# Kernel tuning notes

Measured on AMD Instinct MI355X. Metric: run time of the kernel, lower is better.

Reference implementation:

```python
import jax, jax.numpy as jnp
import numpy as np

N_NODES = 50000
N_EDGES = 1000000
N_QUERY = 100000
NUM_FEATURES = 256
HIDDEN = 256
LABEL_DIM = 2


def glorot(key, shape):
    lim = float(np.sqrt(6.0 / (shape[0] + shape[1])))
    return jax.random.uniform(key, shape, jnp.float32, -lim, lim)


def setup_inputs() -> dict:
    key = jax.random.key(0)
    ks = jax.random.split(key, 8)
    x = jax.random.normal(ks[0], (N_NODES, NUM_FEATURES), jnp.float32)
    edge_index = jax.random.randint(ks[1], (2, N_EDGES), 0, N_NODES)
    query_edges = jax.random.randint(ks[2], (N_QUERY, 2), 0, N_NODES)
    edge_weight = jax.random.uniform(ks[3], (N_EDGES,), jnp.float32)
    W1 = glorot(ks[4], (NUM_FEATURES, HIDDEN))
    b1 = jnp.zeros((HIDDEN,), jnp.float32)
    W2 = glorot(ks[5], (HIDDEN, HIDDEN))
    b2 = jnp.zeros((HIDDEN,), jnp.float32)
    Wl = glorot(ks[6], (2 * HIDDEN, LABEL_DIM))
    bl = jnp.zeros((LABEL_DIM,), jnp.float32)
    return {"x": x, "edge_index": edge_index, "query_edges": query_edges,
            "edge_weight": edge_weight, "W1": W1, "b1": b1, "W2": W2,
            "b2": b2, "Wl": Wl, "bl": bl}


def digcn_conv(x, edge_index, edge_weight, W, b):
    # x: [N, F_in] -> h: [N, F_out]; propagate: out[dst] += w_e * h[src]
    h = x @ W
    src, dst = edge_index[0], edge_index[1]
    msg = h[src] * edge_weight[:, None]            # [E, F_out]
    agg = jax.ops.segment_sum(msg, dst, num_segments=x.shape[0])
    return agg + b


def reference(x, edge_index, query_edges, edge_weight, W1, b1, W2, b2, Wl, bl):
    h = jax.nn.relu(digcn_conv(x, edge_index, edge_weight, W1, b1))
    # dropout is identity at eval time
    h = digcn_conv(h, edge_index, edge_weight, W2, b2)
    q = jnp.concatenate((h[query_edges[:, 0]], h[query_edges[:, 1]]), axis=-1)
    logits = q @ Wl + bl
    return jax.nn.log_softmax(logits, axis=1)
```

## Files before the change

kernel.cpp:

```cpp
#include <hip/hip_runtime.h>
#include <hip/hip_bf16.h>
#include <math.h>

typedef __bf16 bf16;
typedef __bf16 v8bf __attribute__((ext_vector_type(8)));
typedef __bf16 v4bf __attribute__((ext_vector_type(4)));
typedef float  v4f  __attribute__((ext_vector_type(4)));

#define FDIM 256
#define BKT_CAP 8192
#define AROW 264
#define GEMM_BLOCKS 512


__global__ __launch_bounds__(256) void flag_kernel(float* __restrict__ out, int n) {
  int i = blockIdx.x * 256 + threadIdx.x;
  if (i < n) out[i] = 1.0e9f;
}

__global__ __launch_bounds__(256) void k1_prep(const float* __restrict__ W1,
                                               const float* __restrict__ W2,
                                               bf16* __restrict__ Wt1,
                                               bf16* __restrict__ Wt2,
                                               const int* __restrict__ dst,
                                               int* __restrict__ phist,
                                               const float* __restrict__ Wl,
                                               const float* __restrict__ b2,
                                               const float* __restrict__ bl,
                                               float4* __restrict__ V,
                                               float* __restrict__ cc,
                                               int E, int N, int nbkt) {
  __shared__ int h[256];
  __shared__ float sWl[1024];
  __shared__ float red[256];
  int b = blockIdx.x;
  int t = threadIdx.x;
  if (b < 512) {
    const float* W = (b >> 8) ? W2 : W1;
    bf16* Wt = (b >> 8) ? Wt2 : Wt1;
    int k = b & 255;
    Wt[t * FDIM + k] = (bf16)W[k * FDIM + t];
  } else if (b < 768) {
    int pb = b - 512;
    h[t] = 0;
    __syncthreads();
    for (int e = pb * 256 + t; e < E; e += 256 * 256) {
      int d = dst[e];
      d = d < 0 ? 0 : (d >= N ? N - 1 : d);
      atomicAdd(&h[d >> 8], 1);
    }
    __syncthreads();
    phist[pb * 256 + t] = h[t];
  } else {
#pragma unroll
    for (int j = 0; j < 4; ++j) sWl[j * 256 + t] = Wl[j * 256 + t];
    __syncthreads();
    const float* w2row = W2 + (size_t)t * FDIM;
    float4 acc = make_float4(0.f, 0.f, 0.f, 0.f);
    for (int j = 0; j < 256; ++j) {
      float w = w2row[j];
      acc.x += w * sWl[2 * j + 0];
      acc.y += w * sWl[2 * j + 1];
      acc.z += w * sWl[512 + 2 * j + 0];
      acc.w += w * sWl[512 + 2 * j + 1];
    }
    V[t] = acc;
    float bj = b2[t];
    red[t] = bj * (sWl[2 * t + 0] + sWl[512 + 2 * t + 0]);
    __syncthreads();
    if (t == 0) {
      float s = 0.f;
      for (int j = 0; j < 256; ++j) s += red[j];
      cc[0] = s + bl[0];
    }
    __syncthreads();
    red[t] = bj * (sWl[2 * t + 1] + sWl[512 + 2 * t + 1]);
    __syncthreads();
    if (t == 0) {
      float s = 0.f;
      for (int j = 0; j < 256; ++j) s += red[j];
      cc[1] = s + bl[1];
    }
  }
}

__global__ __launch_bounds__(256) void p2_scan(const int* __restrict__ phist,
                                               int* __restrict__ bbase,
                                               int* __restrict__ gcur,
                                               int* __restrict__ offs,
                                               int nbkt, int Nn) {
  __shared__ int wsum[4];
  int t = threadIdx.x, lane = t & 63, wv = t >> 6;
  int v = 0;
  for (int pb = 0; pb < 256; ++pb) v += phist[pb * 256 + t];
  if (t >= nbkt) v = 0;
  int x = v;
#pragma unroll
  for (int d = 1; d < 64; d <<= 1) {
    int y = __shfl_up(x, d, 64);
    if (lane >= d) x += y;
  }
  if (lane == 63) wsum[wv] = x;
  __syncthreads();
  int woff = 0;
  if (wv >= 1) woff += wsum[0];
  if (wv >= 2) woff += wsum[1];
  if (wv >= 3) woff += wsum[2];
  int incl = woff + x;
  int excl = incl - v;
  if (t < nbkt) { bbase[t] = excl; gcur[t] = excl; }
  if (t == 255) {
    bbase[nbkt] = incl;
    offs[Nn] = incl;
  }
}


__device__ inline void stage64(const float* __restrict__ A, bf16* __restrict__ As,
                               int row0, int M, int tid) {
#pragma unroll
  for (int j = 0; j < 8; ++j) {
    int g = j * 2048 + tid * 8;
    int r = g >> 8, c = g & 255;
    int gr = row0 + r; if (gr >= M) gr = M - 1;
    const float* p = A + (size_t)gr * FDIM + c;
    float4 f0 = *reinterpret_cast<const float4*>(p);
    float4 f1 = *reinterpret_cast<const float4*>(p + 4);
    v8bf o;
    o[0] = (bf16)f0.x; o[1] = (bf16)f0.y; o[2] = (bf16)f0.z; o[3] = (bf16)f0.w;
    o[4] = (bf16)f1.x; o[5] = (bf16)f1.y; o[6] = (bf16)f1.z; o[7] = (bf16)f1.w;
    *reinterpret_cast<v8bf*>(As + r * AROW + c) = o;
  }
}

__device__ inline void gemm_body(const float* __restrict__ A, const bf16* __restrict__ Bt,
                                 bf16* __restrict__ C, int M, int bid, int nblocks,
                                 bf16* __restrict__ As) {
  const int K = FDIM, N = FDIM;
  int tid = threadIdx.x;
  int wave = tid >> 6;
  int lane = tid & 63;
  int l15 = lane & 15, quad = lane >> 4;

  v8bf bfr[4][8];
#pragma unroll
  for (int nn = 0; nn < 4; ++nn) {
    const bf16* bp = Bt + (size_t)(wave * 64 + nn * 16 + l15) * K + quad * 8;
#pragma unroll
    for (int kk = 0; kk < 8; ++kk)
      bfr[nn][kk] = *reinterpret_cast<const v8bf*>(bp + kk * 32);
  }

  int ntiles = (M + 63) >> 6;
  for (int tile = bid; tile < ntiles; tile += nblocks) {
    int row0 = tile * 64;
    __syncthreads();
    stage64(A, As, row0, M, tid);
    __syncthreads();

#pragma unroll
    for (int st = 0; st < 4; ++st) {
      v8bf afr[8];
#pragma unroll
      for (int kk = 0; kk < 8; ++kk)
        afr[kk] = *reinterpret_cast<const v8bf*>(As + (st * 16 + l15) * AROW + quad * 8 + kk * 32);

      v4f acc[4];
#pragma unroll
      for (int nn = 0; nn < 4; ++nn) acc[nn] = (v4f){0.f, 0.f, 0.f, 0.f};

#pragma unroll
      for (int kk = 0; kk < 8; ++kk)
#pragma unroll
        for (int nn = 0; nn < 4; ++nn)
          acc[nn] = __builtin_amdgcn_mfma_f32_16x16x32_bf16(afr[kk], bfr[nn][kk], acc[nn], 0, 0, 0);

#pragma unroll
      for (int nn = 0; nn < 4; ++nn)
#pragma unroll
        for (int r = 0; r < 4; ++r) {
          int row = row0 + st * 16 + quad * 4 + r;
          int col = wave * 64 + nn * 16 + l15;
          if (row < M) C[(size_t)row * N + col] = (bf16)acc[nn][r];
        }
    }
  }
}

__device__ inline void p3_body(const int* __restrict__ src, const int* __restrict__ dst,
                               const float* __restrict__ ew, int* __restrict__ gcur,
                               uint2* __restrict__ tmp, int E, int N, int nbkt,
                               int pb, int nblocks, int* h, int* base, int* cnt) {
  int t = threadIdx.x;
  int chunk = (E + nblocks - 1) / nblocks;
  int lo = pb * chunk;
  int hi = lo + chunk; if (hi > E) hi = E;
  h[t] = 0; cnt[t] = 0;
  __syncthreads();
  for (int e = lo + t; e < hi; e += 256) {
    int d = dst[e];
    d = d < 0 ? 0 : (d >= N ? N - 1 : d);
    atomicAdd(&h[d >> 8], 1);
  }
  __syncthreads();
  if (t < nbkt) base[t] = atomicAdd(&gcur[t], h[t]);
  __syncthreads();
  for (int e = lo + t; e < hi; e += 256) {
    int d = dst[e];
    d = d < 0 ? 0 : (d >= N ? N - 1 : d);
    int b = d >> 8;
    int sv = src[e];
    sv = sv < 0 ? 0 : (sv >= N ? N - 1 : sv);
    unsigned int u = __float_as_uint(ew[e]);
    unsigned int wbits = ((u + 0x7FFFu + ((u >> 16) & 1u)) & 0xFFFF0000u);
    unsigned int meta = wbits | (unsigned int)(sv & 0xFFFF);
    int r = atomicAdd(&cnt[b], 1);
    int pos = base[b] + r;
    if (pos >= 0 && pos < E) tmp[pos] = make_uint2(meta, (unsigned int)d);
  }
}

__global__ __launch_bounds__(256, 2) void k3_gemm1_p3(const float* __restrict__ x,
                                                      const bf16* __restrict__ Wt1,
                                                      bf16* __restrict__ bufT, int M,
                                                      const int* __restrict__ src,
                                                      const int* __restrict__ dst,
                                                      const float* __restrict__ ew,
                                                      int* __restrict__ gcur,
                                                      uint2* __restrict__ tmp,
                                                      int E, int N, int nbkt) {
  __shared__ bf16 As[64 * AROW];
  __shared__ int h[256], base[256], cnt[256];
  if (blockIdx.x < GEMM_BLOCKS)
    gemm_body(x, Wt1, bufT, M, blockIdx.x, GEMM_BLOCKS, As);
  else
    p3_body(src, dst, ew, gcur, tmp, E, N, nbkt, blockIdx.x - GEMM_BLOCKS, 256, h, base, cnt);
}

__global__ __launch_bounds__(256) void p4_sort(const uint2* __restrict__ tmp,
                                               const int* __restrict__ bbase,
                                               unsigned int* __restrict__ pmeta,
                                               int* __restrict__ offs,
                                               int Nn, int E) {
  __shared__ uint2 ent[BKT_CAP];
  __shared__ int h2[256], ex2[256], c2[256];
  __shared__ int wsum[4];
  int b = blockIdx.x, t = threadIdx.x, lane = t & 63, wv = t >> 6;
  int s0 = bbase[b], s1 = bbase[b + 1];
  int count = s1 - s0;
  if (count < 0) count = 0;
  if (count > BKT_CAP) count = BKT_CAP;
  for (int i = t; i < count; i += 256) ent[i] = tmp[s0 + i];
  h2[t] = 0; c2[t] = 0;
  __syncthreads();
  for (int i = t; i < count; i += 256) atomicAdd(&h2[ent[i].y & 255u], 1);
  __syncthreads();
  int v = h2[t];
  int x = v;
#pragma unroll
  for (int d = 1; d < 64; d <<= 1) {
    int y = __shfl_up(x, d, 64);
    if (lane >= d) x += y;
  }
  if (lane == 63) wsum[wv] = x;
  __syncthreads();
  int woff = 0;
  if (wv >= 1) woff += wsum[0];
  if (wv >= 2) woff += wsum[1];
  if (wv >= 3) woff += wsum[2];
  int excl = woff + x - v;
  ex2[t] = excl;
  int node = (b << 8) + t;
  if (node < Nn) offs[node] = s0 + excl;
  __syncthreads();
  for (int i = t; i < count; i += 256) {
    int l = (int)(ent[i].y & 255u);
    int r = atomicAdd(&c2[l], 1);
    int pos = s0 + ex2[l] + r;
    if (pos >= 0 && pos < E) pmeta[pos] = ent[i].x;
  }
}

__global__ __launch_bounds__(256) void agg1G(const bf16* __restrict__ T,
                                             const unsigned int* __restrict__ pmeta,
                                             const int* __restrict__ offsets,
                                             const float* __restrict__ bias,
                                             const float4* __restrict__ V,
                                             float4* __restrict__ G, int N, int E) {
  int node = blockIdx.x * 4 + (threadIdx.x >> 6);
  if (node >= N) return;
  int lane = threadIdx.x & 63;
  int f = lane * 4;
  int beg = offsets[node], end = offsets[node + 1];
  beg = beg < 0 ? 0 : (beg > E ? E : beg);
  end = end < beg ? beg : (end > E ? E : end);
  const unsigned int* m = pmeta + beg;
  int cnt = end - beg;

  float a0 = 0.f, a1 = 0.f, a2 = 0.f, a3 = 0.f;
  int p = 0;
  for (; p + 8 <= cnt; p += 8) {
    unsigned int mv[8];
#pragma unroll
    for (int j = 0; j < 8; ++j) mv[j] = m[p + j];
    v4bf tv[8];
#pragma unroll
    for (int j = 0; j < 8; ++j) {
      int s = (int)(mv[j] & 0xFFFFu);
      s = s >= N ? N - 1 : s;
      tv[j] = *reinterpret_cast<const v4bf*>(T + (size_t)s * FDIM + f);
    }
#pragma unroll
    for (int j = 0; j < 8; ++j) {
      float w = __uint_as_float(mv[j] & 0xFFFF0000u);
      a0 += w * (float)tv[j][0];
      a1 += w * (float)tv[j][1];
      a2 += w * (float)tv[j][2];
      a3 += w * (float)tv[j][3];
    }
  }
  for (; p < cnt; ++p) {
    unsigned int mv = m[p];
    int s = (int)(mv & 0xFFFFu);
    s = s >= N ? N - 1 : s;
    float w = __uint_as_float(mv & 0xFFFF0000u);
    v4bf tv = *reinterpret_cast<const v4bf*>(T + (size_t)s * FDIM + f);
    a0 += w * (float)tv[0];
    a1 += w * (float)tv[1];
    a2 += w * (float)tv[2];
    a3 += w * (float)tv[3];
  }
  a0 = fmaxf(a0 + bias[f + 0], 0.f);
  a1 = fmaxf(a1 + bias[f + 1], 0.f);
  a2 = fmaxf(a2 + bias[f + 2], 0.f);
  a3 = fmaxf(a3 + bias[f + 3], 0.f);

  float4 v0 = V[f + 0], v1 = V[f + 1], v2 = V[f + 2], v3 = V[f + 3];
  float gx = a0 * v0.x + a1 * v1.x + a2 * v2.x + a3 * v3.x;
  float gy = a0 * v0.y + a1 * v1.y + a2 * v2.y + a3 * v3.y;
  float gz = a0 * v0.z + a1 * v1.z + a2 * v2.z + a3 * v3.z;
  float gw = a0 * v0.w + a1 * v1.w + a2 * v2.w + a3 * v3.w;
#pragma unroll
  for (int d = 32; d > 0; d >>= 1) {
    gx += __shfl_down(gx, d, 64);
    gy += __shfl_down(gy, d, 64);
    gz += __shfl_down(gz, d, 64);
    gw += __shfl_down(gw, d, 64);
  }
  if (lane == 0) G[node] = make_float4(gx, gy, gz, gw);
}

__global__ __launch_bounds__(256) void aggP(const float4* __restrict__ G,
                                            const unsigned int* __restrict__ pmeta,
                                            const int* __restrict__ offsets,
                                            float4* __restrict__ P, int N, int E) {
  int node = blockIdx.x * 256 + threadIdx.x;
  if (node >= N) return;
  int beg = offsets[node], end = offsets[node + 1];
  beg = beg < 0 ? 0 : (beg > E ? E : beg);
  end = end < beg ? beg : (end > E ? E : end);
  float ax = 0.f, ay = 0.f, az = 0.f, aw = 0.f;
  int p = beg;
  for (; p + 4 <= end; p += 4) {
    unsigned int m0 = pmeta[p + 0], m1 = pmeta[p + 1], m2 = pmeta[p + 2], m3 = pmeta[p + 3];
    int s0 = (int)(m0 & 0xFFFFu); s0 = s0 >= N ? N - 1 : s0;
    int s1 = (int)(m1 & 0xFFFFu); s1 = s1 >= N ? N - 1 : s1;
    int s2 = (int)(m2 & 0xFFFFu); s2 = s2 >= N ? N - 1 : s2;
    int s3 = (int)(m3 & 0xFFFFu); s3 = s3 >= N ? N - 1 : s3;
    float4 g0 = G[s0], g1 = G[s1], g2 = G[s2], g3 = G[s3];
    float w0 = __uint_as_float(m0 & 0xFFFF0000u);
    float w1 = __uint_as_float(m1 & 0xFFFF0000u);
    float w2 = __uint_as_float(m2 & 0xFFFF0000u);
    float w3 = __uint_as_float(m3 & 0xFFFF0000u);
    ax += w0 * g0.x + w1 * g1.x + w2 * g2.x + w3 * g3.x;
    ay += w0 * g0.y + w1 * g1.y + w2 * g2.y + w3 * g3.y;
    az += w0 * g0.z + w1 * g1.z + w2 * g2.z + w3 * g3.z;
    aw += w0 * g0.w + w1 * g1.w + w2 * g2.w + w3 * g3.w;
  }
  for (; p < end; ++p) {
    unsigned int mm = pmeta[p];
    int s = (int)(mm & 0xFFFFu); s = s >= N ? N - 1 : s;
    float w = __uint_as_float(mm & 0xFFFF0000u);
    float4 g = G[s];
    ax += w * g.x; ay += w * g.y; az += w * g.z; aw += w * g.w;
  }
  P[node] = make_float4(ax, ay, az, aw);
}

__global__ __launch_bounds__(256) void query_small(const int* __restrict__ qe,
                                                   const float4* __restrict__ P,
                                                   const float* __restrict__ cc,
                                                   float* __restrict__ out, int Q, int N) {
  int q = blockIdx.x * 256 + threadIdx.x;
  if (q >= Q) return;
  int n0 = qe[2 * q + 0]; n0 = n0 < 0 ? 0 : (n0 >= N ? N - 1 : n0);
  int n1 = qe[2 * q + 1]; n1 = n1 < 0 ? 0 : (n1 >= N ? N - 1 : n1);
  float4 p0 = P[n0];
  float4 p1 = P[n1];
  float l0 = p0.x + p1.z + cc[0];
  float l1 = p0.y + p1.w + cc[1];
  float m = fmaxf(l0, l1);
  float lse = m + logf(expf(l0 - m) + expf(l1 - m));
  out[2 * q + 0] = l0 - lse;
  out[2 * q + 1] = l1 - lse;
}


extern "C" void kernel_launch(void* const* d_in, const int* in_sizes, int n_in,
                              void* d_out, int out_size, void* d_ws, size_t ws_size,
                              hipStream_t stream) {
  const float* x  = (const float*)d_in[0];
  const int*   ei = (const int*)d_in[1];
  const int*   qe = (const int*)d_in[2];
  const float* ew = (const float*)d_in[3];
  const float* W1 = (const float*)d_in[4];
  const float* b1 = (const float*)d_in[5];
  const float* W2 = (const float*)d_in[6];
  const float* b2 = (const float*)d_in[7];
  const float* Wl = (const float*)d_in[8];
  const float* bl = (const float*)d_in[9];

  int N = in_sizes[0] / FDIM;
  int E = in_sizes[1] / 2;
  int Q = in_sizes[2] / 2;
  const int* srcv = ei;
  const int* dstv = ei + E;
  int nbkt = (N + 255) >> 8;

  size_t off = 0;
  auto alloc = [&](size_t bytes) -> void* {
    void* p = (char*)d_ws + off;
    off += (bytes + 255) & ~(size_t)255;
    return p;
  };
  bf16* bufT  = (bf16*)alloc((size_t)N * FDIM * 2);
  uint2* tmp  = (uint2*)alloc((size_t)E * 8);
  bf16* Wt1   = (bf16*)alloc((size_t)FDIM * FDIM * 2);
  bf16* Wt2   = (bf16*)alloc((size_t)FDIM * FDIM * 2);
  int* offs   = (int*)alloc((size_t)(N + 1) * 4);
  unsigned int* pmeta = (unsigned int*)alloc((size_t)E * 4);
  float4* G   = (float4*)alloc((size_t)N * 16);
  float4* P   = (float4*)alloc((size_t)N * 16);
  float4* V   = (float4*)alloc(256 * 16);
  float* cc   = (float*)alloc(2 * 4);
  int* phist  = (int*)alloc(256 * 256 * 4);
  int* bbase  = (int*)alloc(257 * 4);
  int* gcur   = (int*)alloc(256 * 4);

  if (off > ws_size) {
    flag_kernel<<<(out_size + 255) / 256, 256, 0, stream>>>((float*)d_out, out_size);
    return;
  }

  k1_prep<<<769, 256, 0, stream>>>(W1, W2, Wt1, Wt2, dstv, phist, Wl, b2, bl, V, cc,
                                   E, N, nbkt);
  p2_scan<<<1, 256, 0, stream>>>(phist, bbase, gcur, offs, nbkt, N);
  k3_gemm1_p3<<<GEMM_BLOCKS + 256, 256, 0, stream>>>(x, Wt1, bufT, N,
                                                     srcv, dstv, ew, gcur, tmp, E, N, nbkt);
  p4_sort<<<nbkt, 256, 0, stream>>>(tmp, bbase, pmeta, offs, N, E);

  agg1G<<<(N + 3) / 4, 256, 0, stream>>>(bufT, pmeta, offs, b1, V, G, N, E);

  aggP<<<(N + 255) / 256, 256, 0, stream>>>(G, pmeta, offs, P, N, E);

  query_small<<<(Q + 255) / 256, 256, 0, stream>>>(qe, P, cc, (float*)d_out, Q, N);
}
```

Before: 250.9 us.

## Split agg1G by feature slices with persistent waves and atomic partial reductions

The first-layer aggregation is restructured so each block handles a 32-feature slice (8 slices) over a grid-strided set of nodes. Within a wave, four lane groups split the node's edge list and are combined with shuffles, and partial projections onto V are accumulated into G with float atomics. G is now zeroed inside p4_sort. The intent is to make gathers from the feature table hit a smaller working set per slice, which improves cache locality, and to add edge-level parallelism for each node. In exchange, metadata is re-read 8 times, each node needs four global atomics per slice, and the source-index clamp is dropped.

```diff
diff --git a/kernel.cpp b/kernel.cpp
--- a/kernel.cpp
+++ b/kernel.cpp
@@ -5,6 +5,7 @@
 typedef __bf16 bf16;
 typedef __bf16 v8bf __attribute__((ext_vector_type(8)));
 typedef __bf16 v4bf __attribute__((ext_vector_type(4)));
+typedef __bf16 v2bf __attribute__((ext_vector_type(2)));
 typedef float  v4f  __attribute__((ext_vector_type(4)));
 
 #define FDIM 256
@@ -241,11 +242,14 @@
                                                const int* __restrict__ bbase,
                                                unsigned int* __restrict__ pmeta,
                                                int* __restrict__ offs,
+                                               float4* __restrict__ G,
                                                int Nn, int E) {
   __shared__ uint2 ent[BKT_CAP];
   __shared__ int h2[256], ex2[256], c2[256];
   __shared__ int wsum[4];
   int b = blockIdx.x, t = threadIdx.x, lane = t & 63, wv = t >> 6;
+  int nodez = (b << 8) + t;
+  if (nodez < Nn) G[nodez] = make_float4(0.f, 0.f, 0.f, 0.f);
   int s0 = bbase[b], s1 = bbase[b + 1];
   int count = s1 - s0;
   if (count < 0) count = 0;
@@ -287,67 +291,84 @@
                                              const float* __restrict__ bias,
                                              const float4* __restrict__ V,
                                              float4* __restrict__ G, int N, int E) {
-  int node = blockIdx.x * 4 + (threadIdx.x >> 6);
-  if (node >= N) return;
+  int slice = blockIdx.x & 7;
+  int chunk = blockIdx.x >> 3;
+  int nchunk = gridDim.x >> 3;
+  int wv = threadIdx.x >> 6;
   int lane = threadIdx.x & 63;
-  int f = lane * 4;
-  int beg = offsets[node], end = offsets[node + 1];
-  beg = beg < 0 ? 0 : (beg > E ? E : beg);
-  end = end < beg ? beg : (end > E ? E : end);
-  const unsigned int* m = pmeta + beg;
-  int cnt = end - beg;
-
-  float a0 = 0.f, a1 = 0.f, a2 = 0.f, a3 = 0.f;
-  int p = 0;
-  for (; p + 8 <= cnt; p += 8) {
-    unsigned int mv[8];
-#pragma unroll
-    for (int j = 0; j < 8; ++j) mv[j] = m[p + j];
-    v4bf tv[8];
-#pragma unroll
-    for (int j = 0; j < 8; ++j) {
-      int s = (int)(mv[j] & 0xFFFFu);
-      s = s >= N ? N - 1 : s;
-      tv[j] = *reinterpret_cast<const v4bf*>(T + (size_t)s * FDIM + f);
-    }
-#pragma unroll
-    for (int j = 0; j < 8; ++j) {
-      float w = __uint_as_float(mv[j] & 0xFFFF0000u);
-      a0 += w * (float)tv[j][0];
-      a1 += w * (float)tv[j][1];
-      a2 += w * (float)tv[j][2];
-      a3 += w * (float)tv[j][3];
-    }
-  }
-  for (; p < cnt; ++p) {
-    unsigned int mv = m[p];
-    int s = (int)(mv & 0xFFFFu);
-    s = s >= N ? N - 1 : s;
-    float w = __uint_as_float(mv & 0xFFFF0000u);
-    v4bf tv = *reinterpret_cast<const v4bf*>(T + (size_t)s * FDIM + f);
-    a0 += w * (float)tv[0];
-    a1 += w * (float)tv[1];
-    a2 += w * (float)tv[2];
-    a3 += w * (float)tv[3];
-  }
-  a0 = fmaxf(a0 + bias[f + 0], 0.f);
-  a1 = fmaxf(a1 + bias[f + 1], 0.f);
-  a2 = fmaxf(a2 + bias[f + 2], 0.f);
-  a3 = fmaxf(a3 + bias[f + 3], 0.f);
-
-  float4 v0 = V[f + 0], v1 = V[f + 1], v2 = V[f + 2], v3 = V[f + 3];
-  float gx = a0 * v0.x + a1 * v1.x + a2 * v2.x + a3 * v3.x;
-  float gy = a0 * v0.y + a1 * v1.y + a2 * v2.y + a3 * v3.y;
-  float gz = a0 * v0.z + a1 * v1.z + a2 * v2.z + a3 * v3.z;
-  float gw = a0 * v0.w + a1 * v1.w + a2 * v2.w + a3 * v3.w;
-#pragma unroll
-  for (int d = 32; d > 0; d >>= 1) {
-    gx += __shfl_down(gx, d, 64);
-    gy += __shfl_down(gy, d, 64);
-    gz += __shfl_down(gz, d, 64);
-    gw += __shfl_down(gw, d, 64);
-  }
-  if (lane == 0) G[node] = make_float4(gx, gy, gz, gw);
+  int grp = lane >> 4;
+  int l16 = lane & 15;
+  int f = slice * 32 + l16 * 2;
+  const bf16* Tf = T + f;
+
+  float bb0 = bias[f], bb1 = bias[f + 1];
+  float4 v0 = V[f], v1 = V[f + 1];
+
+  int wid = chunk * 4 + wv;
+  int stride = nchunk * 4;
+  for (int node = wid; node < N; node += stride) {
+    int nb = __builtin_amdgcn_readfirstlane(node);
+    int beg = offsets[nb], end = offsets[nb + 1];
+    beg = beg < 0 ? 0 : (beg > E ? E : beg);
+    end = end < beg ? beg : (end > E ? E : end);
+    int cnt = end - beg;
+    int g0 = (cnt * grp) >> 2;
+    int g1 = (cnt * (grp + 1)) >> 2;
+    const unsigned int* m = pmeta + beg;
+
+    float a0 = 0.f, a1 = 0.f;
+    int p = g0;
+    for (; p + 4 <= g1; p += 4) {
+      unsigned int m0 = __builtin_nontemporal_load(&m[p + 0]);
+      unsigned int m1 = __builtin_nontemporal_load(&m[p + 1]);
+      unsigned int m2 = __builtin_nontemporal_load(&m[p + 2]);
+      unsigned int m3 = __builtin_nontemporal_load(&m[p + 3]);
+      v2bf t0 = *reinterpret_cast<const v2bf*>(Tf + ((size_t)(m0 & 0xFFFFu) << 8));
+      v2bf t1 = *reinterpret_cast<const v2bf*>(Tf + ((size_t)(m1 & 0xFFFFu) << 8));
+      v2bf t2 = *reinterpret_cast<const v2bf*>(Tf + ((size_t)(m2 & 0xFFFFu) << 8));
+      v2bf t3 = *reinterpret_cast<const v2bf*>(Tf + ((size_t)(m3 & 0xFFFFu) << 8));
+      float w0 = __uint_as_float(m0 & 0xFFFF0000u);
+      float w1 = __uint_as_float(m1 & 0xFFFF0000u);
+      float w2 = __uint_as_float(m2 & 0xFFFF0000u);
+      float w3 = __uint_as_float(m3 & 0xFFFF0000u);
+      a0 += w0 * (float)t0[0]; a1 += w0 * (float)t0[1];
+      a0 += w1 * (float)t1[0]; a1 += w1 * (float)t1[1];
+      a0 += w2 * (float)t2[0]; a1 += w2 * (float)t2[1];
+      a0 += w3 * (float)t3[0]; a1 += w3 * (float)t3[1];
+    }
+    for (; p < g1; ++p) {
+      unsigned int mv = __builtin_nontemporal_load(&m[p]);
+      float w = __uint_as_float(mv & 0xFFFF0000u);
+      v2bf tv = *reinterpret_cast<const v2bf*>(Tf + ((size_t)(mv & 0xFFFFu) << 8));
+      a0 += w * (float)tv[0];
+      a1 += w * (float)tv[1];
+    }
+
+    a0 += __shfl_xor(a0, 16, 64); a0 += __shfl_xor(a0, 32, 64);
+    a1 += __shfl_xor(a1, 16, 64); a1 += __shfl_xor(a1, 32, 64);
+
+    float r0 = fmaxf(a0 + bb0, 0.f);
+    float r1 = fmaxf(a1 + bb1, 0.f);
+
+    float gx = r0 * v0.x + r1 * v1.x;
+    float gy = r0 * v0.y + r1 * v1.y;
+    float gz = r0 * v0.z + r1 * v1.z;
+    float gw = r0 * v0.w + r1 * v1.w;
+#pragma unroll
+    for (int d = 1; d < 16; d <<= 1) {
+      gx += __shfl_xor(gx, d, 64);
+      gy += __shfl_xor(gy, d, 64);
+      gz += __shfl_xor(gz, d, 64);
+      gw += __shfl_xor(gw, d, 64);
+    }
+    if (lane == 0) {
+      float* gp = reinterpret_cast<float*>(&G[node]);
+      atomicAdd(gp + 0, gx);
+      atomicAdd(gp + 1, gy);
+      atomicAdd(gp + 2, gz);
+      atomicAdd(gp + 3, gw);
+    }
+  }
 }
 
 __global__ __launch_bounds__(256) void aggP(const float4* __restrict__ G,
@@ -457,9 +478,9 @@
   p2_scan<<<1, 256, 0, stream>>>(phist, bbase, gcur, offs, nbkt, N);
   k3_gemm1_p3<<<GEMM_BLOCKS + 256, 256, 0, stream>>>(x, Wt1, bufT, N,
                                                      srcv, dstv, ew, gcur, tmp, E, N, nbkt);
-  p4_sort<<<nbkt, 256, 0, stream>>>(tmp, bbase, pmeta, offs, N, E);
-
-  agg1G<<<(N + 3) / 4, 256, 0, stream>>>(bufT, pmeta, offs, b1, V, G, N, E);
+  p4_sort<<<nbkt, 256, 0, stream>>>(tmp, bbase, pmeta, offs, G, N, E);
+
+  agg1G<<<2048, 256, 0, stream>>>(bufT, pmeta, offs, b1, V, G, N, E);
 
   aggP<<<(N + 255) / 256, 256, 0, stream>>>(G, pmeta, offs, P, N, E);
 
```

Result: slower. 371.5 us (+48.1%).
